# Optimization experiments

Hardware: AMD Instinct MI355X
Metric: run time of the kernel (lower is better)

## Reference

```python
import jax, jax.numpy as jnp
import numpy as np

B, S, E, HD = 32, 1024, 768, 64
NUM_IMAGE_PATCHES = 49


def setup_inputs() -> dict:
    key = jax.random.key(0)
    ks = jax.random.split(key, 9)
    w = 0.02
    return {
        "decoder_sequence": jax.random.normal(ks[0], (B, S, E), dtype=jnp.float32),
        "Wq": jax.random.normal(ks[1], (E, HD), dtype=jnp.float32) * w,
        "bq": jnp.zeros((HD,), dtype=jnp.float32),
        "Wk": jax.random.normal(ks[2], (E, HD), dtype=jnp.float32) * w,
        "bk": jnp.zeros((HD,), dtype=jnp.float32),
        "Wv": jax.random.normal(ks[3], (E, HD), dtype=jnp.float32) * w,
        "bv": jnp.zeros((HD,), dtype=jnp.float32),
        "input_sequence_length": 975,
        "padding_mask": jax.random.randint(ks[4], (B, 1, S), 0, 2).astype(bool),
    }


def reference(decoder_sequence, Wq, bq, Wk, bk, Wv, bv, input_sequence_length, padding_mask):
    # single-head projections: [B,S,E] @ [E,HD] -> [B,S,HD]
    Q = decoder_sequence @ Wq + bq
    K = decoder_sequence @ Wk + bk
    V = decoder_sequence @ Wv + bv

    scores = jnp.einsum('bid,bjd->bij', Q, K) / jnp.sqrt(jnp.float32(HD))

    # mask: image-patch rows (i < 49) fully unmasked; text region is causal
    # (mask[49:,49:] = triu(-inf, diag=1)), i.e. -inf where i >= 49 and j > i.
    i = jnp.arange(S)[:, None]
    j = jnp.arange(S)[None, :]
    causal_bad = (i >= NUM_IMAGE_PATCHES) & (j > i)  # [S,S]
    scores = jnp.where(causal_bad[None, :, :], -jnp.inf, scores)

    # padding mask on keys, broadcast over queries: [B,1,S] -> [B,S,S]
    scores = jnp.where(padding_mask, -jnp.inf, scores)

    A = jax.nn.softmax(scores, axis=-1)
    H = jnp.einsum('bij,bjd->bid', A, V)
    return H
```

## Files before the change

kernel.cpp:

```cpp
#include <hip/hip_runtime.h>
#include <stdint.h>
#include <stddef.h>


typedef __attribute__((ext_vector_type(8))) short bf16x8;
typedef __attribute__((ext_vector_type(4))) float f32x4;

#define NIP 49
#define QSCALE 0.18033688011112042f

#define GLDS16(g, l)                                      \
  __builtin_amdgcn_global_load_lds(                       \
      (const __attribute__((address_space(1))) void*)(g), \
      (__attribute__((address_space(3))) void*)(l), 16, 0, 0)

__device__ __forceinline__ short f2b(float f) {
  union { float f; uint32_t u; } c; c.f = f;
  uint32_t u = c.u;
  uint32_t r = (u + 0x7fffu + ((u >> 16) & 1u)) >> 16;
  return (short)(uint16_t)r;
}

__device__ __forceinline__ uint32_t pk2(float lo, float hi) {
  uint32_t r;
  asm("v_cvt_pk_bf16_f32 %0, %1, %2" : "=v"(r) : "v"(lo), "v"(hi));
  return r;
}

__global__ __launch_bounds__(256) void wt_kernel(
    const float* __restrict__ Wq, const float* __restrict__ Wk,
    const float* __restrict__ Wv, const int* __restrict__ pad,
    short* __restrict__ Wt, float* __restrict__ padneg) {
  int idx = blockIdx.x * 256 + threadIdx.x;
  int n = idx / 768;
  int k = idx - n * 768;
  const float* W = (n < 64) ? Wq : (n < 128) ? Wk : Wv;
  Wt[idx] = f2b(W[(size_t)k * 64 + (n & 63)]);
  if (idx < 32768) padneg[idx] = pad[idx] ? -16384.f : 0.f;
}

__global__ __launch_bounds__(256, 2) void proj_kernel(
    const float* __restrict__ X, const float* __restrict__ bq,
    const float* __restrict__ bk, const float* __restrict__ bv,
    const short* __restrict__ Wt, short* __restrict__ Qg,
    short* __restrict__ Kg, short* __restrict__ Vt) {
  __shared__ short lX[2][2][64][32];
  __shared__ short lW[2][2][192][32];
  const int tid = threadIdx.x;
  const int wid = tid >> 6, lane = tid & 63;
  const int l15 = lane & 15, q4 = lane >> 4;
  const int r0 = blockIdx.x * 64;

  float4 rx[4];
  auto xload = [&](int kb) {
#pragma unroll
    for (int i = 0; i < 4; ++i) {
      const int xi = tid + i * 256;
      rx[i] = *(const float4*)(X + (size_t)(r0 + (xi >> 4)) * 768 + kb + (xi & 15) * 4);
    }
  };
  auto xstage = [&](int buf) {
#pragma unroll
    for (int i = 0; i < 4; ++i) {
      const int xi = tid + i * 256;
      uint2 s;
      s.x = pk2(rx[i].x, rx[i].y);
      s.y = pk2(rx[i].z, rx[i].w);
      *(uint2*)&lX[buf][(xi & 15) >> 3][xi >> 4][(xi & 7) * 4] = s;
    }
  };
  const int wr = lane >> 2, wc = (lane & 3) * 8;
  auto wlds = [&](int buf, int kb) {
#pragma unroll
    for (int i = 0; i < 6; ++i) {
      const int fi = wid * 6 + i;
      const int j = fi >> 1, ks = fi & 1;
      GLDS16(Wt + (size_t)(j * 16 + wr) * 768 + kb + ks * 32 + wc,
             &lW[buf][ks][j * 16][0]);
    }
  };

  f32x4 acc[12];
#pragma unroll
  for (int c = 0; c < 12; ++c) acc[c] = (f32x4){0.f, 0.f, 0.f, 0.f};

  xload(0);
  wlds(0, 0);
  xstage(0);
  __syncthreads();

#pragma unroll
  for (int st = 0; st < 12; ++st) {
    const int cur = st & 1;
    if (st + 1 < 12) {
      xload((st + 1) * 64);
      wlds(cur ^ 1, (st + 1) * 64);
    }
#pragma unroll
    for (int ks = 0; ks < 2; ++ks) {
      bf16x8 a = *(const bf16x8*)&lX[cur][ks][wid * 16 + l15][q4 * 8];
#pragma unroll
      for (int c = 0; c < 12; ++c) {
        bf16x8 bw = *(const bf16x8*)&lW[cur][ks][c * 16 + l15][q4 * 8];
        acc[c] = __builtin_amdgcn_mfma_f32_16x16x32_bf16(a, bw, acc[c], 0, 0, 0);
      }
    }
    if (st + 1 < 12) xstage(cur ^ 1);
    __syncthreads();
  }

  const int b = r0 >> 10, s0 = r0 & 1023;
#pragma unroll
  for (int c = 0; c < 12; ++c) {
    const int mtx = c >> 2;
    const int h = (c & 3) * 16 + l15;
    if (mtx < 2) {
      const float bias = (mtx == 0 ? bq : bk)[h];
      short* op = (mtx == 0) ? Qg : Kg;
#pragma unroll
      for (int rr = 0; rr < 4; ++rr) {
        int row = r0 + wid * 16 + q4 * 4 + rr;
        float v = acc[c][rr] + bias;
        if (mtx == 0) v *= QSCALE;
        op[(size_t)row * 64 + h] = f2b(v);
      }
    } else {
      const float bias = bv[h];
      uint2 sv;
      sv.x = pk2(acc[c][0] + bias, acc[c][1] + bias);
      sv.y = pk2(acc[c][2] + bias, acc[c][3] + bias);
      *(uint2*)(Vt + ((size_t)(b * 64 + h) << 10) + s0 + wid * 16 + q4 * 4) = sv;
    }
  }
}

__global__ __launch_bounds__(256, 2) void attn_kernel(
    const short* __restrict__ Qg, const short* __restrict__ Kg,
    const short* __restrict__ Vt, const float* __restrict__ padneg,
    float* __restrict__ out) {
  __shared__ short lK[2][2][128][32];
  __shared__ short lV[2][4][64][32];
  __shared__ short lOnes[16][32];

  const int b = blockIdx.x;
  const int level = blockIdx.y;
  const int t = (level == 0) ? 0 : 16 - level;
  const int tid = threadIdx.x;
  const int wid = tid >> 6, lane = tid & 63;
  const int l15 = lane & 15, q4 = lane >> 4;
  const int qs = t * 64;
  const size_t base = (size_t)b * 1024;
  const int nkt = (t == 0) ? 8 : (t / 2 + 1);

  {
    int i0 = tid, i1 = tid + 256;
    ((short*)lOnes)[i0] = ((i0 >> 5) == 0) ? (short)0x3F80 : (short)0;
    if (i1 < 512) ((short*)lOnes)[i1] = ((i1 >> 5) == 0) ? (short)0x3F80 : (short)0;
  }

  const short* qrow = Qg + (base + qs + wid * 16 + l15) * 64;
  bf16x8 bq0 = *(const bf16x8*)(qrow + q4 * 8);
  bf16x8 bq1 = *(const bf16x8*)(qrow + 32 + q4 * 8);
  const int qi = qs + wid * 16 + l15;

  const int sr = lane >> 2, sc = (lane & 3) * 8;
  auto wlds_tile = [&](int buf, int kt) {
    const int kb = kt * 128;
#pragma unroll
    for (int i = 0; i < 4; ++i) {
      const int dh = i & 1, krow = wid * 32 + (i >> 1) * 16;
      GLDS16(Kg + (base + kb + krow + sr) * 64 + dh * 32 + sc,
             &lK[buf][dh][krow][0]);
    }
#pragma unroll
    for (int kq = 0; kq < 4; ++kq) {
      GLDS16(Vt + ((size_t)(b * 64 + wid * 16 + sr) << 10) + kb + kq * 32 + sc,
             &lV[buf][kq][wid * 16][0]);
    }
  };

  float4 pnv[8];
  auto pnload = [&](int kt) {
#pragma unroll
    for (int c = 0; c < 8; ++c)
      pnv[c] = *(const float4*)(padneg + base + kt * 128 + c * 16 + q4 * 4);
  };

  pnload(0);
  wlds_tile(0, 0);
  __syncthreads();

  f32x4 o[5];
#pragma unroll
  for (int c = 0; c < 5; ++c) o[c] = (f32x4){0.f, 0.f, 0.f, 0.f};

  for (int kt = 0; kt < nkt; ++kt) {
    const int cur = kt & 1;
    const int kb = kt * 128;

    f32x4 s4[8];
#pragma unroll
    for (int c = 0; c < 8; ++c)
      s4[c] = (f32x4){pnv[c].x, pnv[c].y, pnv[c].z, pnv[c].w};

    if (kt + 1 < nkt) {
      wlds_tile(cur ^ 1, kt + 1);
      pnload(kt + 1);
    }

#pragma unroll
    for (int c = 0; c < 8; ++c) {
      bf16x8 a0 = *(const bf16x8*)&lK[cur][0][c * 16 + l15][q4 * 8];
      s4[c] = __builtin_amdgcn_mfma_f32_16x16x32_bf16(a0, bq0, s4[c], 0, 0, 0);
      bf16x8 a1 = *(const bf16x8*)&lK[cur][1][c * 16 + l15][q4 * 8];
      s4[c] = __builtin_amdgcn_mfma_f32_16x16x32_bf16(a1, bq1, s4[c], 0, 0, 0);
    }

    const bool diag = (t == 0) ? (kt == 0) : (kt == nkt - 1);
    const bool img = (t == 0 && kt > 0);
#pragma unroll
    for (int c = 0; c < 8; ++c) {
#pragma unroll
      for (int rr = 0; rr < 4; ++rr) {
        float pv = exp2f(fminf(s4[c][rr], 80.f));
        if (diag) {
          int j = kb + c * 16 + q4 * 4 + rr;
          if (qi >= NIP && j > qi) pv = 0.f;
        }
        if (img) {
          if (qi >= NIP) pv = 0.f;
        }
        s4[c][rr] = pv;
      }
    }

#pragma unroll
    for (int m = 0; m < 4; ++m) {
      uint32_t w0 = pk2(s4[2 * m][0], s4[2 * m][1]);
      uint32_t w1 = pk2(s4[2 * m][2], s4[2 * m][3]);
      uint32_t w2 = pk2(s4[2 * m + 1][0], s4[2 * m + 1][1]);
      uint32_t w3 = pk2(s4[2 * m + 1][2], s4[2 * m + 1][3]);
      asm("v_permlane32_swap_b32 %0, %1" : "+v"(w0), "+v"(w2));
      asm("v_permlane32_swap_b32 %0, %1" : "+v"(w1), "+v"(w3));
      asm("v_permlane16_swap_b32 %0, %1" : "+v"(w0), "+v"(w2));
      asm("v_permlane16_swap_b32 %0, %1" : "+v"(w1), "+v"(w3));
      union { uint32_t u[4]; bf16x8 v; } af;
      af.u[0] = w0; af.u[1] = w1; af.u[2] = w2; af.u[3] = w3;
#pragma unroll
      for (int c = 0; c < 5; ++c) {
        bf16x8 bv = (c < 4) ? *(const bf16x8*)&lV[cur][m][c * 16 + l15][q4 * 8]
                            : *(const bf16x8*)&lOnes[l15][q4 * 8];
        o[c] = __builtin_amdgcn_mfma_f32_16x16x32_bf16(af.v, bv, o[c], 0, 0, 0);
      }
    }
    __syncthreads();
  }

#pragma unroll
  for (int rr = 0; rr < 4; ++rr) {
    float l = __shfl(o[4][rr], lane & 48, 64);
    const float inv = (l > 0.f) ? 1.0f / l : 0.f;
    const size_t row = base + qs + wid * 16 + q4 * 4 + rr;
#pragma unroll
    for (int c = 0; c < 4; ++c)
      out[row * 64 + c * 16 + l15] = o[c][rr] * inv;
  }
}

extern "C" void kernel_launch(void* const* d_in, const int* in_sizes, int n_in,
                              void* d_out, int out_size, void* d_ws, size_t ws_size,
                              hipStream_t stream) {
  const float* X  = (const float*)d_in[0];
  const float* Wq = (const float*)d_in[1];
  const float* bq = (const float*)d_in[2];
  const float* Wk = (const float*)d_in[3];
  const float* bk = (const float*)d_in[4];
  const float* Wv = (const float*)d_in[5];
  const float* bv = (const float*)d_in[6];
  const int* pad  = (const int*)d_in[8];
  float* out = (float*)d_out;

  short* Qg = (short*)d_ws;
  short* Kg = Qg + 32768 * 64;
  short* Vt = Kg + 32768 * 64;
  short* Wt = Vt + 32768 * 64;
  float* padneg = (float*)(Wt + 147456);

  wt_kernel<<<576, 256, 0, stream>>>(Wq, Wk, Wv, pad, Wt, padneg);
  proj_kernel<<<512, 256, 0, stream>>>(X, bq, bk, bv, Wt, Qg, Kg, Vt);
  attn_kernel<<<dim3(32, 16), 256, 0, stream>>>(Qg, Kg, Vt, padneg, out);
}
```

Baseline: 199.6 us.

## Load X fragments directly to registers with two-stage prefetch and swizzled W LDS

The projection kernel no longer stages X through shared memory. Each lane loads its MFMA A-fragment rows from global memory two steps ahead and converts them to bf16 in registers. The W tile in LDS gets an XOR swizzle to cut bank conflicts, and explicit waitcnt/barrier calls replace __syncthreads. Launch bounds rise to 3 blocks per CU. The cost is more register pressure and X global loads with a less coalesced access pattern.

```diff
diff --git a/kernel.cpp b/kernel.cpp
--- a/kernel.cpp
+++ b/kernel.cpp
@@ -39,43 +39,45 @@
   if (idx < 32768) padneg[idx] = pad[idx] ? -16384.f : 0.f;
 }
 
-__global__ __launch_bounds__(256, 2) void proj_kernel(
+__global__ __launch_bounds__(256, 3) void proj_kernel(
     const float* __restrict__ X, const float* __restrict__ bq,
     const float* __restrict__ bk, const float* __restrict__ bv,
     const short* __restrict__ Wt, short* __restrict__ Qg,
     short* __restrict__ Kg, short* __restrict__ Vt) {
-  __shared__ short lX[2][2][64][32];
   __shared__ short lW[2][2][192][32];
   const int tid = threadIdx.x;
   const int wid = tid >> 6, lane = tid & 63;
   const int l15 = lane & 15, q4 = lane >> 4;
   const int r0 = blockIdx.x * 64;
-
-  float4 rx[4];
-  auto xload = [&](int kb) {
-#pragma unroll
-    for (int i = 0; i < 4; ++i) {
-      const int xi = tid + i * 256;
-      rx[i] = *(const float4*)(X + (size_t)(r0 + (xi >> 4)) * 768 + kb + (xi & 15) * 4);
-    }
-  };
-  auto xstage = [&](int buf) {
-#pragma unroll
-    for (int i = 0; i < 4; ++i) {
-      const int xi = tid + i * 256;
-      uint2 s;
-      s.x = pk2(rx[i].x, rx[i].y);
-      s.y = pk2(rx[i].z, rx[i].w);
-      *(uint2*)&lX[buf][(xi & 15) >> 3][xi >> 4][(xi & 7) * 4] = s;
-    }
-  };
-  const int wr = lane >> 2, wc = (lane & 3) * 8;
-  auto wlds = [&](int buf, int kb) {
+  const int sig = (l15 >> 1) & 3;
+
+  const float* xrow = X + (size_t)(r0 + wid * 16 + l15) * 768;
+  float4 xa[2][4];
+  auto xload = [&](int slot, int st) {
+    const int kb = st * 64 + q4 * 8;
+#pragma unroll
+    for (int h = 0; h < 2; ++h) {
+      xa[slot][h * 2 + 0] = *(const float4*)(xrow + kb + h * 32);
+      xa[slot][h * 2 + 1] = *(const float4*)(xrow + kb + h * 32 + 4);
+    }
+  };
+  auto mkfrag = [&](int slot, int h) {
+    union { uint32_t u[4]; bf16x8 v; } r;
+    const float4 a = xa[slot][h * 2], b = xa[slot][h * 2 + 1];
+    r.u[0] = pk2(a.x, a.y); r.u[1] = pk2(a.z, a.w);
+    r.u[2] = pk2(b.x, b.y); r.u[3] = pk2(b.z, b.w);
+    return r.v;
+  };
+
+  const int wr = lane >> 2;
+  const int ws = (((lane & 3) ^ ((wr >> 1) & 3)) * 8);
+  auto wlds = [&](int buf, int st) {
+    const int kb = st * 64;
 #pragma unroll
     for (int i = 0; i < 6; ++i) {
       const int fi = wid * 6 + i;
       const int j = fi >> 1, ks = fi & 1;
-      GLDS16(Wt + (size_t)(j * 16 + wr) * 768 + kb + ks * 32 + wc,
+      GLDS16(Wt + (size_t)(j * 16 + wr) * 768 + kb + ks * 32 + ws,
              &lW[buf][ks][j * 16][0]);
     }
   };
@@ -84,29 +86,38 @@
 #pragma unroll
   for (int c = 0; c < 12; ++c) acc[c] = (f32x4){0.f, 0.f, 0.f, 0.f};
 
-  xload(0);
   wlds(0, 0);
-  xstage(0);
-  __syncthreads();
+  __builtin_amdgcn_sched_barrier(0);
+  xload(0, 0);
+  xload(1, 1);
+  asm volatile("s_waitcnt vmcnt(8) lgkmcnt(0)" ::: "memory");
+  __builtin_amdgcn_s_barrier();
 
 #pragma unroll
   for (int st = 0; st < 12; ++st) {
     const int cur = st & 1;
     if (st + 1 < 12) {
-      xload((st + 1) * 64);
-      wlds(cur ^ 1, (st + 1) * 64);
-    }
+      wlds(cur ^ 1, st + 1);
+      __builtin_amdgcn_sched_barrier(0);
+    }
+    const bf16x8 a0 = mkfrag(cur, 0);
+    const bf16x8 a1 = mkfrag(cur, 1);
+    if (st + 2 < 12) xload(cur, st + 2);
 #pragma unroll
     for (int ks = 0; ks < 2; ++ks) {
-      bf16x8 a = *(const bf16x8*)&lX[cur][ks][wid * 16 + l15][q4 * 8];
+      const bf16x8 a = ks ? a1 : a0;
 #pragma unroll
       for (int c = 0; c < 12; ++c) {
-        bf16x8 bw = *(const bf16x8*)&lW[cur][ks][c * 16 + l15][q4 * 8];
+        const bf16x8 bw =
+            *(const bf16x8*)&lW[cur][ks][c * 16 + l15][(q4 ^ sig) * 8];
         acc[c] = __builtin_amdgcn_mfma_f32_16x16x32_bf16(a, bw, acc[c], 0, 0, 0);
       }
     }
-    if (st + 1 < 12) xstage(cur ^ 1);
-    __syncthreads();
+    if (st + 2 < 12)
+      asm volatile("s_waitcnt vmcnt(4) lgkmcnt(0)" ::: "memory");
+    else
+      asm volatile("s_waitcnt vmcnt(0) lgkmcnt(0)" ::: "memory");
+    __builtin_amdgcn_s_barrier();
   }
 
   const int b = r0 >> 10, s0 = r0 & 1023;
```

After: 198.1 us. Within noise of the previous version (-0.8%).
